# Kernel optimization log

Measured on AMD Instinct MI355X. Metric: run time of the kernel, lower is better.

Reference implementation:

```python
import jax, jax.numpy as jnp
import numpy as np
from jax import lax

DIM = 256
NUM_HEADS = 8
HEAD_DIM = DIM // NUM_HEADS
DN = ('NCHW', 'OIHW', 'NCHW')


def _dsconv(x, dw, dwb, pw, pwb):
    # depthwise 3x3 (groups = C) then pointwise 1x1
    C = x.shape[1]
    y = lax.conv_general_dilated(x, dw, (1, 1), 'SAME',
                                 dimension_numbers=DN,
                                 feature_group_count=C)
    y = y + dwb[None, :, None, None]
    y = lax.conv_general_dilated(y, pw, (1, 1), 'SAME', dimension_numbers=DN)
    return y + pwb[None, :, None, None]


def _to_heads(x):
    # (B, C, H, W) -> (B, nh, HW, hd)
    B, C, H, W = x.shape
    return x.reshape(B, NUM_HEADS, HEAD_DIM, H * W).transpose(0, 1, 3, 2)


def setup_inputs() -> dict:
    key = jax.random.key(0)
    ks = jax.random.split(key, 14)
    B, H, W = 2, 64, 64
    inp = {
        'x': jax.random.normal(ks[0], (B, DIM, H, W), jnp.float32),
        'ctx': jax.random.normal(ks[1], (B, DIM, H, W), jnp.float32),
    }
    i = 2
    for name in ('q', 'k', 'v'):
        inp[f'{name}_dw'] = jax.random.normal(ks[i], (DIM, 1, 3, 3), jnp.float32) * 0.05; i += 1
        inp[f'{name}_dwb'] = jnp.zeros((DIM,), jnp.float32)
        inp[f'{name}_pw'] = jax.random.normal(ks[i], (DIM, DIM, 1, 1), jnp.float32) * 0.05; i += 1
        inp[f'{name}_pwb'] = jnp.zeros((DIM,), jnp.float32)
    return inp


def reference(x, ctx,
              q_dw, q_dwb, q_pw, q_pwb,
              k_dw, k_dwb, k_pw, k_pwb,
              v_dw, v_dwb, v_pw, v_pwb):
    B, C, H, W = x.shape
    scale = HEAD_DIM ** 0.5
    q = _to_heads(_dsconv(x, q_dw, q_dwb, q_pw, q_pwb))    # (B, nh, HW, hd)
    k = _to_heads(_dsconv(ctx, k_dw, k_dwb, k_pw, k_pwb))
    v = _to_heads(_dsconv(ctx, v_dw, v_dwb, v_pw, v_pwb))
    attn = jnp.einsum('bnqd,bnkd->bnqk', q, k) / scale      # (B, nh, HW, HW)
    attn = jax.nn.softmax(attn, axis=-1)
    out = jnp.einsum('bnqk,bnkd->bnqd', attn, v)            # (B, nh, HW, hd)
    out = out.transpose(0, 1, 3, 2).reshape(B, DIM, H * W)  # (B, dim, HW)
    return out
```

## Files before the change

### kernel.cpp

```cpp
#include <hip/hip_runtime.h>
#include <hip/hip_bf16.h>


#define HW 4096
#define CDIM 256
#define SCALE_LOG2E 0.2550348543f

typedef short bf16x8 __attribute__((ext_vector_type(8)));
typedef float f32x4 __attribute__((ext_vector_type(4)));
typedef float f32x16 __attribute__((ext_vector_type(16)));

__device__ inline unsigned short f2bf(float f) {
  unsigned u = __float_as_uint(f);
  u = (u + 0x7fffu + ((u >> 16) & 1u)) >> 16;
  return (unsigned short)u;
}

__device__ inline unsigned cvtpk(float lo, float hi) {
  unsigned r;
  asm("v_cvt_pk_bf16_f32 %0, %1, %2" : "=v"(r) : "v"(lo), "v"(hi));
  return r;
}

__device__ inline float fexp2(float x) {
#if __has_builtin(__builtin_amdgcn_exp2f)
  return __builtin_amdgcn_exp2f(x);
#else
  return exp2f(x);
#endif
}

__device__ inline void plswap(unsigned& a, unsigned& b) {
#if __has_builtin(__builtin_amdgcn_permlane32_swap)
  auto r = __builtin_amdgcn_permlane32_swap((int)a, (int)b, false, false);
  a = (unsigned)r[0];
  b = (unsigned)r[1];
#else
  unsigned as = __shfl_xor((int)a, 32), bs = __shfl_xor((int)b, 32);
  bool hi = (threadIdx.x & 32) != 0;
  unsigned na = hi ? bs : a;
  unsigned nb = hi ? b : as;
  a = na; b = nb;
#endif
}

__global__ __launch_bounds__(256) void dw_all(
    const float* __restrict__ x, const float* __restrict__ ctx,
    const float* __restrict__ qdw, const float* __restrict__ qdwb,
    const float* __restrict__ kdw, const float* __restrict__ kdwb,
    const float* __restrict__ vdw, const float* __restrict__ vdwb,
    unsigned short* __restrict__ tq, unsigned short* __restrict__ tk,
    unsigned short* __restrict__ tv) {
  int gid = blockIdx.x * 256 + threadIdx.x;
  int tt = gid >> 19;
  int r = gid & 524287;
  int q4 = r & 1023;
  int plane = r >> 10;
  int c = plane & 255;
  int w0 = (q4 & 15) * 4, h = q4 >> 4;
  const float* src = (tt == 0 ? x : ctx) + (size_t)plane * HW;
  const float* wc = (tt == 0 ? qdw : (tt == 1 ? kdw : vdw)) + c * 9;
  float bv = (tt == 0 ? qdwb : (tt == 1 ? kdwb : vdwb))[c];
  float acc0 = bv, acc1 = bv, acc2 = bv, acc3 = bv;
#pragma unroll
  for (int kh = 0; kh < 3; ++kh) {
    int hh = h + kh - 1;
    if (hh < 0 || hh > 63) continue;
    const float* row = src + hh * 64 + w0;
    float4 m = *(const float4*)row;
    float lft = (w0 > 0) ? row[-1] : 0.f;
    float rgt = (w0 < 60) ? row[4] : 0.f;
    float e0 = lft, e1 = m.x, e2 = m.y, e3 = m.z, e4 = m.w, e5 = rgt;
    float w_0 = wc[kh * 3 + 0], w_1 = wc[kh * 3 + 1], w_2 = wc[kh * 3 + 2];
    acc0 += w_0 * e0 + w_1 * e1 + w_2 * e2;
    acc1 += w_0 * e1 + w_1 * e2 + w_2 * e3;
    acc2 += w_0 * e2 + w_1 * e3 + w_2 * e4;
    acc3 += w_0 * e3 + w_1 * e4 + w_2 * e5;
  }
  unsigned short* out = (tt == 0 ? tq : (tt == 1 ? tk : tv));
  ushort4 pk = make_ushort4(f2bf(acc0), f2bf(acc1), f2bf(acc2), f2bf(acc3));
  *(ushort4*)(out + (size_t)plane * HW + h * 64 + w0) = pk;
}

__global__ __launch_bounds__(256) void pw_all(
    const unsigned short* __restrict__ tq, const unsigned short* __restrict__ tk,
    const unsigned short* __restrict__ tv,
    const float* __restrict__ qw, const float* __restrict__ qbs,
    const float* __restrict__ kw, const float* __restrict__ kbs,
    const float* __restrict__ vw, const float* __restrict__ vbs,
    unsigned short* __restrict__ Qc, unsigned short* __restrict__ Kc,
    unsigned short* __restrict__ Vc) {
  __shared__ __align__(16) unsigned char Bs[64 * 512];
  int tt = blockIdx.x >> 9;
  int bid = blockIdx.x & 511;
  const unsigned short* t = tt == 0 ? tq : (tt == 1 ? tk : tv);
  const float* w = tt == 0 ? qw : (tt == 1 ? kw : vw);
  const float* bias = tt == 0 ? qbs : (tt == 1 ? kbs : vbs);
  unsigned short* out = tt == 0 ? Qc : (tt == 1 ? Kc : Vc);
  float oscale = tt == 0 ? SCALE_LOG2E : 1.0f;

  int pt = bid & 63, cot = (bid >> 6) & 3, bb = bid >> 8;
  int p0 = pt * 64, co0 = cot * 64;
  int tid = threadIdx.x;
  int wv = tid >> 6, l = tid & 63, lq = l & 15, lg = l >> 4;

  bf16x8 af[8];
  {
    const float* wr = w + (size_t)(co0 + wv * 16 + lq) * 256;
#pragma unroll
    for (int kt = 0; kt < 8; ++kt) {
      float4 a = *(const float4*)(wr + kt * 32 + lg * 8);
      float4 bq = *(const float4*)(wr + kt * 32 + lg * 8 + 4);
      union { unsigned u[4]; bf16x8 v; } cv;
      cv.u[0] = cvtpk(a.x, a.y);  cv.u[1] = cvtpk(a.z, a.w);
      cv.u[2] = cvtpk(bq.x, bq.y); cv.u[3] = cvtpk(bq.z, bq.w);
      af[kt] = cv.v;
    }
  }
  {
    int cb = tid >> 3, po = tid & 7;
    const unsigned short* src = t + (size_t)bb * (CDIM * HW) + (size_t)(cb * 8) * HW + p0 + po * 8;
    uint4 r[8];
#pragma unroll
    for (int i = 0; i < 8; ++i) r[i] = *(const uint4*)(src + (size_t)i * HW);
#pragma unroll
    for (int jj = 0; jj < 8; ++jj) {
      uint4 o;
#pragma unroll
      for (int ww = 0; ww < 4; ++ww) {
        unsigned a = ((const unsigned*)&r[2 * ww])[jj >> 1];
        unsigned b = ((const unsigned*)&r[2 * ww + 1])[jj >> 1];
        unsigned lo = (jj & 1) ? (a >> 16) : (a & 0xffffu);
        unsigned hi = (jj & 1) ? (b & 0xffff0000u) : (b << 16);
        (&o.x)[ww] = lo | hi;
      }
      int p = po * 8 + jj;
      int swz = ((p ^ (p >> 3)) & 7) << 4;
      *(uint4*)(Bs + p * 512 + ((cb * 16) ^ swz)) = o;
    }
  }
  __syncthreads();
  f32x4 acc[4] = {};
#pragma unroll
  for (int nt = 0; nt < 4; ++nt) {
    int p = nt * 16 + lq;
    int swz = ((p ^ (p >> 3)) & 7) << 4;
    const unsigned char* Bp = Bs + p * 512;
#pragma unroll
    for (int kt = 0; kt < 8; ++kt) {
      bf16x8 bf = *(const bf16x8*)(Bp + ((kt * 64 + lg * 16) ^ swz));
      acc[nt] = __builtin_amdgcn_mfma_f32_16x16x32_bf16(af[kt], bf, acc[nt], 0, 0, 0);
    }
  }
  if (tt < 2) {
    int co = co0 + wv * 16 + lg * 4;
    int d0 = co & 31;
    float b0 = bias[co], b1 = bias[co + 1], b2 = bias[co + 2], b3 = bias[co + 3];
    size_t rowb = (size_t)(bb * 8 + (co >> 5)) * HW;
#pragma unroll
    for (int nt = 0; nt < 4; ++nt) {
      int p = p0 + nt * 16 + lq;
      ushort4 pk = make_ushort4(f2bf((acc[nt][0] + b0) * oscale),
                                f2bf((acc[nt][1] + b1) * oscale),
                                f2bf((acc[nt][2] + b2) * oscale),
                                f2bf((acc[nt][3] + b3) * oscale));
      *(ushort4*)(out + (rowb + p) * 32 + d0) = pk;
    }
  } else {
    int cob = co0 + wv * 16 + lg * 4;
#pragma unroll
    for (int r = 0; r < 4; ++r) {
      float bv = bias[cob + r];
      size_t rb = (size_t)bb * (CDIM * HW) + (size_t)(cob + r) * HW + p0;
#pragma unroll
      for (int nt = 0; nt < 4; ++nt)
        out[rb + nt * 16 + lq] = f2bf(acc[nt][r] + bv);
    }
  }
}

__global__ __launch_bounds__(512, 4) void attn_kernel(
    const unsigned short* __restrict__ Qt, const unsigned short* __restrict__ Kt,
    const unsigned short* __restrict__ Vn, float* __restrict__ out) {
  __shared__ __align__(16) unsigned char lds[38912];
  int bid0 = blockIdx.x;
  int bid = (bid0 & 7) * 64 + (bid0 >> 3);
  int qb = bid & 31, bh = bid >> 5;
  int b = bh >> 3, n = bh & 7;
  int tid = threadIdx.x;
  int l = tid & 63, wv = tid >> 6;
  int qg = wv & 3, ks = wv >> 2;
  int lq = l & 31, hi = l >> 5;

  const unsigned short* Qg = Qt + (size_t)bh * (HW * 32);
  const unsigned short* Kg = Kt + (size_t)bh * (HW * 32);
  const unsigned short* Vg = Vn + (size_t)(b * CDIM + n * 32) * HW;

  int q0 = qb * 128 + qg * 32;
  bf16x8 qfh0 = *(const bf16x8*)(Qg + (size_t)(q0 + lq) * 32 + hi * 8);
  bf16x8 qfh1 = *(const bf16x8*)(Qg + (size_t)(q0 + lq) * 32 + 16 + hi * 8);

  f32x16 O = {};
  float ps = 0.f;

  int ht = tid & 255;
  int krow = ht >> 2, kcol = ht & 3;
  int vrow = ht >> 3, vcol = ht & 7;
  unsigned char* Kb0 = lds + (ks * 2 + 0) * 5120;
  unsigned char* Kb1 = lds + (ks * 2 + 1) * 5120;
  unsigned char* Vb0 = lds + 20480 + (ks * 2 + 0) * 4608;
  unsigned char* Vb1 = lds + 20480 + (ks * 2 + 1) * 4608;
  const uint4* Ksrc = (const uint4*)(Kg + (size_t)(ks * 2048) * 32);
  const unsigned short* Vsrc = Vg + (size_t)vrow * HW + ks * 2048 + vcol * 8;

  uint4 kst = Ksrc[krow * 4 + kcol];
  uint4 vst = *(const uint4*)Vsrc;
  *(uint4*)(Kb0 + krow * 80 + kcol * 16) = kst;
  *(uint4*)(Vb0 + vrow * 144 + vcol * 16) = vst;
  kst = Ksrc[(64 + krow) * 4 + kcol];
  vst = *(const uint4*)(Vsrc + 64);

#pragma unroll 1
  for (int c = 0; c < 32; ++c) {
    __syncthreads();
    unsigned char* Kcur = (c & 1) ? Kb1 : Kb0;
    unsigned char* Vcur = (c & 1) ? Vb1 : Vb0;
    if (c < 31) {
      unsigned char* Kn = (c & 1) ? Kb0 : Kb1;
      unsigned char* Vw = (c & 1) ? Vb0 : Vb1;
      *(uint4*)(Kn + krow * 80 + kcol * 16) = kst;
      *(uint4*)(Vw + vrow * 144 + vcol * 16) = vst;
      if (c < 30) {
        kst = Ksrc[((c + 2) * 64 + krow) * 4 + kcol];
        vst = *(const uint4*)(Vsrc + (c + 2) * 64);
      }
    }
#pragma unroll
    for (int t2 = 0; t2 < 2; ++t2) {
      const unsigned char* Krow = Kcur + (t2 * 32 + lq) * 80 + hi * 16;
      bf16x8 kfa = *(const bf16x8*)(Krow);
      bf16x8 kfb = *(const bf16x8*)(Krow + 32);
      f32x16 zz = {};
      __builtin_amdgcn_s_setprio(1);
      f32x16 st = __builtin_amdgcn_mfma_f32_32x32x16_bf16(kfa, qfh0, zz, 0, 0, 0);
      st = __builtin_amdgcn_mfma_f32_32x32x16_bf16(kfb, qfh1, st, 0, 0, 0);
      __builtin_amdgcn_s_setprio(0);
      float p[16];
#pragma unroll
      for (int r = 0; r < 16; ++r) p[r] = fexp2(st[r]);
      float s0 = (p[0] + p[1]) + (p[2] + p[3]);
      float s1 = (p[4] + p[5]) + (p[6] + p[7]);
      float s2 = (p[8] + p[9]) + (p[10] + p[11]);
      float s3 = (p[12] + p[13]) + (p[14] + p[15]);
      ps += (s0 + s1) + (s2 + s3);
      unsigned u0 = cvtpk(p[0], p[1]),  u1 = cvtpk(p[2], p[3]);
      unsigned u2 = cvtpk(p[4], p[5]),  u3 = cvtpk(p[6], p[7]);
      unsigned u4 = cvtpk(p[8], p[9]),  u5 = cvtpk(p[10], p[11]);
      unsigned u6 = cvtpk(p[12], p[13]), u7 = cvtpk(p[14], p[15]);
      plswap(u0, u2);
      plswap(u1, u3);
      plswap(u4, u6);
      plswap(u5, u7);
      union { unsigned w[4]; bf16x8 v; } A0, A1;
      A0.w[0] = u0; A0.w[1] = u1; A0.w[2] = u2; A0.w[3] = u3;
      A1.w[0] = u4; A1.w[1] = u5; A1.w[2] = u6; A1.w[3] = u7;
      const unsigned char* Vrow = Vcur + lq * 144 + t2 * 64;
      bf16x8 vf0 = *(const bf16x8*)(Vrow + hi * 16);
      bf16x8 vf1 = *(const bf16x8*)(Vrow + 32 + hi * 16);
      __builtin_amdgcn_s_setprio(1);
      O = __builtin_amdgcn_mfma_f32_32x32x16_bf16(A0.v, vf0, O, 0, 0, 0);
      O = __builtin_amdgcn_mfma_f32_32x32x16_bf16(A1.v, vf1, O, 0, 0, 0);
      __builtin_amdgcn_s_setprio(0);
    }
  }

  ps += __shfl_xor(ps, 32);
  __syncthreads();
  float* Ox = (float*)lds;
  float* SumX = (float*)(lds + 16896);
  if (ks == 1) {
    float* Or = Ox + qg * (32 * 33) + lq * 33;
#pragma unroll
    for (int rr = 0; rr < 4; ++rr) {
      float4 vv = {O[rr * 4 + 0], O[rr * 4 + 1], O[rr * 4 + 2], O[rr * 4 + 3]};
      *(float4*)(Or + 8 * rr + 4 * hi) = vv;
    }
    if (hi == 0) SumX[qg * 32 + lq] = ps;
  }
  __syncthreads();
  if (ks == 0) {
    const float* Or = Ox + qg * (32 * 33) + lq * 33;
    float rtot = ps + SumX[qg * 32 + lq];
    float rv = 1.0f / rtot;
    size_t ob = ((size_t)(b * CDIM) + n * 32 + lq) * HW;
#pragma unroll
    for (int rr = 0; rr < 4; ++rr) {
      int qlb = 8 * rr + 4 * hi;
      float4 part = *(const float4*)(Or + qlb);
      float4 res;
#pragma unroll
      for (int j = 0; j < 4; ++j) {
        float sq = __int_as_float(
            __builtin_amdgcn_ds_bpermute((qlb + j) * 4, __float_as_int(rv)));
        (&res.x)[j] = (O[rr * 4 + j] + (&part.x)[j]) * sq;
      }
      *(float4*)(out + ob + q0 + qlb) = res;
    }
  }
}

extern "C" void kernel_launch(void* const* d_in, const int* in_sizes, int n_in,
                              void* d_out, int out_size, void* d_ws, size_t ws_size,
                              hipStream_t stream) {
  const float* x   = (const float*)d_in[0];
  const float* ctx = (const float*)d_in[1];
  const float* q_dw  = (const float*)d_in[2];
  const float* q_dwb = (const float*)d_in[3];
  const float* q_pw  = (const float*)d_in[4];
  const float* q_pwb = (const float*)d_in[5];
  const float* k_dw  = (const float*)d_in[6];
  const float* k_dwb = (const float*)d_in[7];
  const float* k_pw  = (const float*)d_in[8];
  const float* k_pwb = (const float*)d_in[9];
  const float* v_dw  = (const float*)d_in[10];
  const float* v_dwb = (const float*)d_in[11];
  const float* v_pw  = (const float*)d_in[12];
  const float* v_pwb = (const float*)d_in[13];

  const size_t N = (size_t)2 * CDIM * HW;
  unsigned short* Qc = (unsigned short*)d_ws;
  unsigned short* Kc = Qc + N;
  unsigned short* Vc = Kc + N;
  unsigned short* tv = Vc + N;
  unsigned short* tq = (unsigned short*)d_out;
  unsigned short* tk = tq + N;

  dw_all<<<6144, 256, 0, stream>>>(x, ctx, q_dw, q_dwb, k_dw, k_dwb, v_dw, v_dwb,
                                   tq, tk, tv);
  pw_all<<<1536, 256, 0, stream>>>(tq, tk, tv, q_pw, q_pwb, k_pw, k_pwb,
                                   v_pw, v_pwb, Qc, Kc, Vc);
  attn_kernel<<<512, 512, 0, stream>>>(Qc, Kc, Vc, (float*)d_out);
}
```

Before: 91.46 us.

## Share ctx loads for K/V depthwise and unroll attention loop by two

The depthwise kernel now computes K and V depthwise outputs from a single load of the ctx stencil, which cuts the grid from three passes to two and removes redundant ctx reads. The attention loop is manually unrolled by two with fixed double-buffer pointers, so the per-iteration buffer selection goes away. The PV accumulation is split into two independent accumulators to break the MFMA dependency chain. The row-sum reduction uses packed float2 adds. In exchange, register pressure rises (extra accumulator, more dw live values).

Result: faster. 85.61 us (-6.4%).

```diff
diff --git a/kernel.cpp b/kernel.cpp
--- a/kernel.cpp
+++ b/kernel.cpp
@@ -7,6 +7,7 @@
 #define SCALE_LOG2E 0.2550348543f
 
 typedef short bf16x8 __attribute__((ext_vector_type(8)));
+typedef float f32x2 __attribute__((ext_vector_type(2)));
 typedef float f32x4 __attribute__((ext_vector_type(4)));
 typedef float f32x16 __attribute__((ext_vector_type(16)));
 
@@ -52,34 +53,65 @@
     unsigned short* __restrict__ tq, unsigned short* __restrict__ tk,
     unsigned short* __restrict__ tv) {
   int gid = blockIdx.x * 256 + threadIdx.x;
-  int tt = gid >> 19;
+  int pass = gid >> 19;
   int r = gid & 524287;
   int q4 = r & 1023;
   int plane = r >> 10;
   int c = plane & 255;
   int w0 = (q4 & 15) * 4, h = q4 >> 4;
-  const float* src = (tt == 0 ? x : ctx) + (size_t)plane * HW;
-  const float* wc = (tt == 0 ? qdw : (tt == 1 ? kdw : vdw)) + c * 9;
-  float bv = (tt == 0 ? qdwb : (tt == 1 ? kdwb : vdwb))[c];
-  float acc0 = bv, acc1 = bv, acc2 = bv, acc3 = bv;
+  const float* src = (pass ? ctx : x) + (size_t)plane * HW;
+
+  float e[3][6];
 #pragma unroll
   for (int kh = 0; kh < 3; ++kh) {
     int hh = h + kh - 1;
-    if (hh < 0 || hh > 63) continue;
-    const float* row = src + hh * 64 + w0;
-    float4 m = *(const float4*)row;
-    float lft = (w0 > 0) ? row[-1] : 0.f;
-    float rgt = (w0 < 60) ? row[4] : 0.f;
-    float e0 = lft, e1 = m.x, e2 = m.y, e3 = m.z, e4 = m.w, e5 = rgt;
-    float w_0 = wc[kh * 3 + 0], w_1 = wc[kh * 3 + 1], w_2 = wc[kh * 3 + 2];
-    acc0 += w_0 * e0 + w_1 * e1 + w_2 * e2;
-    acc1 += w_0 * e1 + w_1 * e2 + w_2 * e3;
-    acc2 += w_0 * e2 + w_1 * e3 + w_2 * e4;
-    acc3 += w_0 * e3 + w_1 * e4 + w_2 * e5;
-  }
-  unsigned short* out = (tt == 0 ? tq : (tt == 1 ? tk : tv));
-  ushort4 pk = make_ushort4(f2bf(acc0), f2bf(acc1), f2bf(acc2), f2bf(acc3));
-  *(ushort4*)(out + (size_t)plane * HW + h * 64 + w0) = pk;
+    if (hh < 0 || hh > 63) {
+#pragma unroll
+      for (int j = 0; j < 6; ++j) e[kh][j] = 0.f;
+    } else {
+      const float* row = src + hh * 64 + w0;
+      float4 m = *(const float4*)row;
+      e[kh][0] = (w0 > 0) ? row[-1] : 0.f;
+      e[kh][1] = m.x; e[kh][2] = m.y; e[kh][3] = m.z; e[kh][4] = m.w;
+      e[kh][5] = (w0 < 60) ? row[4] : 0.f;
+    }
+  }
+  size_t obase = (size_t)plane * HW + h * 64 + w0;
+  if (pass == 0) {
+    const float* wc = qdw + c * 9;
+    float bv = qdwb[c];
+    float a0 = bv, a1 = bv, a2 = bv, a3 = bv;
+#pragma unroll
+    for (int kh = 0; kh < 3; ++kh) {
+      float w_0 = wc[kh * 3], w_1 = wc[kh * 3 + 1], w_2 = wc[kh * 3 + 2];
+      a0 += w_0 * e[kh][0] + w_1 * e[kh][1] + w_2 * e[kh][2];
+      a1 += w_0 * e[kh][1] + w_1 * e[kh][2] + w_2 * e[kh][3];
+      a2 += w_0 * e[kh][2] + w_1 * e[kh][3] + w_2 * e[kh][4];
+      a3 += w_0 * e[kh][3] + w_1 * e[kh][4] + w_2 * e[kh][5];
+    }
+    *(ushort4*)(tq + obase) = make_ushort4(f2bf(a0), f2bf(a1), f2bf(a2), f2bf(a3));
+  } else {
+    const float* wk = kdw + c * 9;
+    const float* wvv = vdw + c * 9;
+    float bk = kdwb[c], bv2 = vdwb[c];
+    float k0 = bk, k1 = bk, k2 = bk, k3 = bk;
+    float v0 = bv2, v1 = bv2, v2 = bv2, v3 = bv2;
+#pragma unroll
+    for (int kh = 0; kh < 3; ++kh) {
+      float kw0 = wk[kh * 3], kw1 = wk[kh * 3 + 1], kw2 = wk[kh * 3 + 2];
+      float vw0 = wvv[kh * 3], vw1 = wvv[kh * 3 + 1], vw2 = wvv[kh * 3 + 2];
+      k0 += kw0 * e[kh][0] + kw1 * e[kh][1] + kw2 * e[kh][2];
+      k1 += kw0 * e[kh][1] + kw1 * e[kh][2] + kw2 * e[kh][3];
+      k2 += kw0 * e[kh][2] + kw1 * e[kh][3] + kw2 * e[kh][4];
+      k3 += kw0 * e[kh][3] + kw1 * e[kh][4] + kw2 * e[kh][5];
+      v0 += vw0 * e[kh][0] + vw1 * e[kh][1] + vw2 * e[kh][2];
+      v1 += vw0 * e[kh][1] + vw1 * e[kh][2] + vw2 * e[kh][3];
+      v2 += vw0 * e[kh][2] + vw1 * e[kh][3] + vw2 * e[kh][4];
+      v3 += vw0 * e[kh][3] + vw1 * e[kh][4] + vw2 * e[kh][5];
+    }
+    *(ushort4*)(tk + obase) = make_ushort4(f2bf(k0), f2bf(k1), f2bf(k2), f2bf(k3));
+    *(ushort4*)(tv + obase) = make_ushort4(f2bf(v0), f2bf(v1), f2bf(v2), f2bf(v3));
+  }
 }
 
 __global__ __launch_bounds__(256) void pw_all(
@@ -179,6 +211,56 @@
   }
 }
 
+struct AttnState {
+  bf16x8 qfh0, qfh1;
+  f32x16 OA, OB, ZZ;
+  float ps;
+  int lq, hi;
+};
+
+__device__ inline void attn_compute(AttnState& S, const unsigned char* Kcur,
+                                    const unsigned char* Vcur) {
+#pragma unroll
+  for (int t2 = 0; t2 < 2; ++t2) {
+    const unsigned char* Krow = Kcur + (t2 * 32 + S.lq) * 80 + S.hi * 16;
+    bf16x8 kfa = *(const bf16x8*)(Krow);
+    bf16x8 kfb = *(const bf16x8*)(Krow + 32);
+    __builtin_amdgcn_s_setprio(1);
+    f32x16 st = __builtin_amdgcn_mfma_f32_32x32x16_bf16(kfa, S.qfh0, S.ZZ, 0, 0, 0);
+    st = __builtin_amdgcn_mfma_f32_32x32x16_bf16(kfb, S.qfh1, st, 0, 0, 0);
+    __builtin_amdgcn_s_setprio(0);
+    float p[16];
+#pragma unroll
+    for (int r = 0; r < 16; ++r) p[r] = fexp2(st[r]);
+    f32x2 a0 = {p[0], p[1]},  a1 = {p[2], p[3]};
+    f32x2 a2 = {p[4], p[5]},  a3 = {p[6], p[7]};
+    f32x2 a4 = {p[8], p[9]},  a5 = {p[10], p[11]};
+    f32x2 a6 = {p[12], p[13]}, a7 = {p[14], p[15]};
+    f32x2 b0 = a0 + a1, b1 = a2 + a3, b2 = a4 + a5, b3 = a6 + a7;
+    f32x2 c0 = b0 + b1, c1 = b2 + b3;
+    f32x2 d0 = c0 + c1;
+    S.ps += d0[0] + d0[1];
+    unsigned u0 = cvtpk(p[0], p[1]),  u1 = cvtpk(p[2], p[3]);
+    unsigned u2 = cvtpk(p[4], p[5]),  u3 = cvtpk(p[6], p[7]);
+    unsigned u4 = cvtpk(p[8], p[9]),  u5 = cvtpk(p[10], p[11]);
+    unsigned u6 = cvtpk(p[12], p[13]), u7 = cvtpk(p[14], p[15]);
+    plswap(u0, u2);
+    plswap(u1, u3);
+    plswap(u4, u6);
+    plswap(u5, u7);
+    union { unsigned w[4]; bf16x8 v; } A0, A1;
+    A0.w[0] = u0; A0.w[1] = u1; A0.w[2] = u2; A0.w[3] = u3;
+    A1.w[0] = u4; A1.w[1] = u5; A1.w[2] = u6; A1.w[3] = u7;
+    const unsigned char* Vrow = Vcur + S.lq * 144 + t2 * 64;
+    bf16x8 vf0 = *(const bf16x8*)(Vrow + S.hi * 16);
+    bf16x8 vf1 = *(const bf16x8*)(Vrow + 32 + S.hi * 16);
+    __builtin_amdgcn_s_setprio(1);
+    S.OA = __builtin_amdgcn_mfma_f32_32x32x16_bf16(A0.v, vf0, S.OA, 0, 0, 0);
+    S.OB = __builtin_amdgcn_mfma_f32_32x32x16_bf16(A1.v, vf1, S.OB, 0, 0, 0);
+    __builtin_amdgcn_s_setprio(0);
+  }
+}
+
 __global__ __launch_bounds__(512, 4) void attn_kernel(
     const unsigned short* __restrict__ Qt, const unsigned short* __restrict__ Kt,
     const unsigned short* __restrict__ Vn, float* __restrict__ out) {
@@ -190,18 +272,19 @@
   int tid = threadIdx.x;
   int l = tid & 63, wv = tid >> 6;
   int qg = wv & 3, ks = wv >> 2;
-  int lq = l & 31, hi = l >> 5;
+
+  AttnState S;
+  S.lq = l & 31; S.hi = l >> 5;
+  S.OA = (f32x16){}; S.OB = (f32x16){}; S.ZZ = (f32x16){};
+  S.ps = 0.f;
 
   const unsigned short* Qg = Qt + (size_t)bh * (HW * 32);
   const unsigned short* Kg = Kt + (size_t)bh * (HW * 32);
   const unsigned short* Vg = Vn + (size_t)(b * CDIM + n * 32) * HW;
 
   int q0 = qb * 128 + qg * 32;
-  bf16x8 qfh0 = *(const bf16x8*)(Qg + (size_t)(q0 + lq) * 32 + hi * 8);
-  bf16x8 qfh1 = *(const bf16x8*)(Qg + (size_t)(q0 + lq) * 32 + 16 + hi * 8);
-
-  f32x16 O = {};
-  float ps = 0.f;
+  S.qfh0 = *(const bf16x8*)(Qg + (size_t)(q0 + S.lq) * 32 + S.hi * 8);
+  S.qfh1 = *(const bf16x8*)(Qg + (size_t)(q0 + S.lq) * 32 + 16 + S.hi * 8);
 
   int ht = tid & 255;
   int krow = ht >> 2, kcol = ht & 3;
@@ -210,70 +293,43 @@
   unsigned char* Kb1 = lds + (ks * 2 + 1) * 5120;
   unsigned char* Vb0 = lds + 20480 + (ks * 2 + 0) * 4608;
   unsigned char* Vb1 = lds + 20480 + (ks * 2 + 1) * 4608;
+  unsigned char* Kw0 = Kb0 + krow * 80 + kcol * 16;
+  unsigned char* Kw1 = Kb1 + krow * 80 + kcol * 16;
+  unsigned char* Vw0 = Vb0 + vrow * 144 + vcol * 16;
+  unsigned char* Vw1 = Vb1 + vrow * 144 + vcol * 16;
   const uint4* Ksrc = (const uint4*)(Kg + (size_t)(ks * 2048) * 32);
   const unsigned short* Vsrc = Vg + (size_t)vrow * HW + ks * 2048 + vcol * 8;
 
   uint4 kst = Ksrc[krow * 4 + kcol];
   uint4 vst = *(const uint4*)Vsrc;
-  *(uint4*)(Kb0 + krow * 80 + kcol * 16) = kst;
-  *(uint4*)(Vb0 + vrow * 144 + vcol * 16) = vst;
+  *(uint4*)Kw0 = kst;
+  *(uint4*)Vw0 = vst;
   kst = Ksrc[(64 + krow) * 4 + kcol];
   vst = *(const uint4*)(Vsrc + 64);
 
 #pragma unroll 1
-  for (int c = 0; c < 32; ++c) {
+  for (int c = 0; c < 32; c += 2) {
     __syncthreads();
-    unsigned char* Kcur = (c & 1) ? Kb1 : Kb0;
-    unsigned char* Vcur = (c & 1) ? Vb1 : Vb0;
-    if (c < 31) {
-      unsigned char* Kn = (c & 1) ? Kb0 : Kb1;
-      unsigned char* Vw = (c & 1) ? Vb0 : Vb1;
-      *(uint4*)(Kn + krow * 80 + kcol * 16) = kst;
-      *(uint4*)(Vw + vrow * 144 + vcol * 16) = vst;
-      if (c < 30) {
-        kst = Ksrc[((c + 2) * 64 + krow) * 4 + kcol];
-        vst = *(const uint4*)(Vsrc + (c + 2) * 64);
-      }
-    }
-#pragma unroll
-    for (int t2 = 0; t2 < 2; ++t2) {
-      const unsigned char* Krow = Kcur + (t2 * 32 + lq) * 80 + hi * 16;
-      bf16x8 kfa = *(const bf16x8*)(Krow);
-      bf16x8 kfb = *(const bf16x8*)(Krow + 32);
-      f32x16 zz = {};
-      __builtin_amdgcn_s_setprio(1);
-      f32x16 st = __builtin_amdgcn_mfma_f32_32x32x16_bf16(kfa, qfh0, zz, 0, 0, 0);
-      st = __builtin_amdgcn_mfma_f32_32x32x16_bf16(kfb, qfh1, st, 0, 0, 0);
-      __builtin_amdgcn_s_setprio(0);
-      float p[16];
-#pragma unroll
-      for (int r = 0; r < 16; ++r) p[r] = fexp2(st[r]);
-      float s0 = (p[0] + p[1]) + (p[2] + p[3]);
-      float s1 = (p[4] + p[5]) + (p[6] + p[7]);
-      float s2 = (p[8] + p[9]) + (p[10] + p[11]);
-      float s3 = (p[12] + p[13]) + (p[14] + p[15]);
-      ps += (s0 + s1) + (s2 + s3);
-      unsigned u0 = cvtpk(p[0], p[1]),  u1 = cvtpk(p[2], p[3]);
-      unsigned u2 = cvtpk(p[4], p[5]),  u3 = cvtpk(p[6], p[7]);
-      unsigned u4 = cvtpk(p[8], p[9]),  u5 = cvtpk(p[10], p[11]);
-      unsigned u6 = cvtpk(p[12], p[13]), u7 = cvtpk(p[14], p[15]);
-      plswap(u0, u2);
-      plswap(u1, u3);
-      plswap(u4, u6);
-      plswap(u5, u7);
-      union { unsigned w[4]; bf16x8 v; } A0, A1;
-      A0.w[0] = u0; A0.w[1] = u1; A0.w[2] = u2; A0.w[3] = u3;
-      A1.w[0] = u4; A1.w[1] = u5; A1.w[2] = u6; A1.w[3] = u7;
-      const unsigned char* Vrow = Vcur + lq * 144 + t2 * 64;
-      bf16x8 vf0 = *(const bf16x8*)(Vrow + hi * 16);
-      bf16x8 vf1 = *(const bf16x8*)(Vrow + 32 + hi * 16);
-      __builtin_amdgcn_s_setprio(1);
-      O = __builtin_amdgcn_mfma_f32_32x32x16_bf16(A0.v, vf0, O, 0, 0, 0);
-      O = __builtin_amdgcn_mfma_f32_32x32x16_bf16(A1.v, vf1, O, 0, 0, 0);
-      __builtin_amdgcn_s_setprio(0);
-    }
-  }
-
+    *(uint4*)Kw1 = kst;
+    *(uint4*)Vw1 = vst;
+    if (c < 30) {
+      kst = Ksrc[((c + 2) * 64 + krow) * 4 + kcol];
+      vst = *(const uint4*)(Vsrc + (c + 2) * 64);
+    }
+    attn_compute(S, Kb0, Vb0);
+    __syncthreads();
+    if (c < 30) {
+      *(uint4*)Kw0 = kst;
+      *(uint4*)Vw0 = vst;
+      kst = Ksrc[((c + 3) * 64 + krow) * 4 + kcol];
+      vst = *(const uint4*)(Vsrc + (c + 3) * 64);
+    }
+    attn_compute(S, Kb1, Vb1);
+  }
+
+  f32x16 O = S.OA + S.OB;
+  float ps = S.ps;
+  int lq = S.lq, hi = S.hi;
   ps += __shfl_xor(ps, 32);
   __syncthreads();
   float* Ox = (float*)lds;
@@ -335,7 +391,7 @@
   unsigned short* tq = (unsigned short*)d_out;
   unsigned short* tk = tq + N;
 
-  dw_all<<<6144, 256, 0, stream>>>(x, ctx, q_dw, q_dwb, k_dw, k_dwb, v_dw, v_dwb,
+  dw_all<<<4096, 256, 0, stream>>>(x, ctx, q_dw, q_dwb, k_dw, k_dwb, v_dw, v_dwb,
                                    tq, tk, tv);
   pw_all<<<1536, 256, 0, stream>>>(tq, tk, tv, q_pw, q_pwb, k_pw, k_pwb,
                                    v_pw, v_pwb, Qc, Kc, Vc);
```
